# Kernel optimization log

Measured on AMD Instinct MI355X. Metric: run time of the kernel, lower is better.

Reference implementation:

```python
import jax, jax.numpy as jnp
import numpy as np
from jax import lax

B, T, D, V, S = 128, 512, 256, 4096, 512

def setup_inputs() -> dict:
    key = jax.random.key(0)
    ks = jax.random.split(key, 12)
    scale = 1.0 / np.sqrt(D)  # PyTorch RNN default init: U(-1/sqrt(H), 1/sqrt(H))
    inp = {
        "input_ids": jax.random.randint(ks[0], (B, T), 0, V),
        "emb": jax.random.normal(ks[1], (V, D), dtype=jnp.float32) * 0.02,
        "W_ih0": jax.random.uniform(ks[2], (D, D), jnp.float32, -scale, scale),
        "W_hh0": jax.random.uniform(ks[3], (D, D), jnp.float32, -scale, scale),
        "b_ih0": jax.random.uniform(ks[4], (D,), jnp.float32, -scale, scale),
        "b_hh0": jax.random.uniform(ks[5], (D,), jnp.float32, -scale, scale),
        "W_ih1": jax.random.uniform(ks[6], (D, D), jnp.float32, -scale, scale),
        "W_hh1": jax.random.uniform(ks[7], (D, D), jnp.float32, -scale, scale),
        "b_ih1": jax.random.uniform(ks[8], (D,), jnp.float32, -scale, scale),
        "b_hh1": jax.random.uniform(ks[9], (D,), jnp.float32, -scale, scale),
        "W_head": jax.random.normal(ks[10], (S, D), dtype=jnp.float32) * np.sqrt(2.0 / (S + D)),
    }
    return inp

def _rnn_layer(x, W_ih, W_hh, b_ih, b_hh):
    # x: (B, T, D). Elman: h_t = tanh(W_ih x_t + b_ih + W_hh h_{t-1} + b_hh)
    pre = jnp.einsum('btd,hd->bth', x, W_ih) + (b_ih + b_hh)  # batched input GEMM
    def step(h, p):
        h = jnp.tanh(p + h @ W_hh.T)
        return h, h
    h0 = jnp.zeros((x.shape[0], W_hh.shape[0]), dtype=x.dtype)
    _, ys = lax.scan(step, h0, pre.transpose(1, 0, 2))  # scan over T
    return ys.transpose(1, 0, 2)  # (B, T, D)

def reference(input_ids, emb, W_ih0, W_hh0, b_ih0, b_hh0, W_ih1, W_hh1, b_ih1, b_hh1, W_head):
    x = emb[input_ids]                       # (B, T, D); dropout is identity at eval
    h1 = _rnn_layer(x, W_ih0, W_hh0, b_ih0, b_hh0)
    h2 = _rnn_layer(h1, W_ih1, W_hh1, b_ih1, b_hh1)
    logits = jnp.einsum('btd,sd->bts', h2, W_head)  # (B, T, S), head has no bias
    return logits
```

## Files before the change

kernel.cpp:

```cpp
#include <hip/hip_runtime.h>
#include <cstdint>
#include <cstddef>

#define D_DIM 256
#define T_DIM 512
#define B_DIM 128
#define S_DIM 512

typedef __attribute__((ext_vector_type(8))) short short8;
typedef __attribute__((ext_vector_type(4))) float f32x4;

__device__ inline unsigned short f2bf(float x) {
    unsigned u = __builtin_bit_cast(unsigned, x);
    unsigned r = (u + 0x7fffu + ((u >> 16) & 1u)) >> 16;
    return (unsigned short)r;
}
__device__ inline float bf2f(unsigned short b) {
    unsigned u = ((unsigned)b) << 16;
    return __builtin_bit_cast(float, u);
}
__device__ inline float fast_tanh(float x) {
    float ax = __builtin_fabsf(x);
    float e  = __expf(-2.0f * ax);
    float r  = (1.0f - e) * __builtin_amdgcn_rcpf(1.0f + e);
    return __builtin_copysignf(r, x);
}

__device__ inline void split4(float4 v, uint2& hi, uint2& lo) {
    unsigned u0 = __builtin_bit_cast(unsigned, v.x);
    unsigned u1 = __builtin_bit_cast(unsigned, v.y);
    unsigned u2 = __builtin_bit_cast(unsigned, v.z);
    unsigned u3 = __builtin_bit_cast(unsigned, v.w);
    hi.x = (u0 >> 16) | (u1 & 0xFFFF0000u);
    hi.y = (u2 >> 16) | (u3 & 0xFFFF0000u);
    float r0 = v.x - __builtin_bit_cast(float, u0 & 0xFFFF0000u);
    float r1 = v.y - __builtin_bit_cast(float, u1 & 0xFFFF0000u);
    float r2 = v.z - __builtin_bit_cast(float, u2 & 0xFFFF0000u);
    float r3 = v.w - __builtin_bit_cast(float, u3 & 0xFFFF0000u);
    lo.x = (__builtin_bit_cast(unsigned, r0) >> 16)
         | (__builtin_bit_cast(unsigned, r1) & 0xFFFF0000u);
    lo.y = (__builtin_bit_cast(unsigned, r2) >> 16)
         | (__builtin_bit_cast(unsigned, r3) & 0xFFFF0000u);
}

__global__ __launch_bounds__(256, 2)
void gemm_bt_mfma(const float* __restrict__ A, const float* __restrict__ Bm,
                  float* __restrict__ C,
                  const float* __restrict__ bias1, const float* __restrict__ bias2,
                  const int* __restrict__ ids, const float* __restrict__ emb,
                  int M, int N, int K)
{
    __shared__ char smem[65536];

    const int tid  = threadIdx.x;
    const int lane = tid & 63;
    const int quad = lane >> 4;
    const int lcol = lane & 15;
    const int wv   = tid >> 6;
    const int wm   = (wv & 1) * 64;
    const int wn   = (wv >> 1) * 64;
    const int m0   = blockIdx.x * 128;
    const int n0   = blockIdx.y * 128;

    const int rm = tid >> 4;
    const int kq = tid & 15;

    const float* arowp[8];
    const float* browp[8];
#pragma unroll
    for (int i = 0; i < 8; ++i) {
        int gm = m0 + rm + i * 16;
        arowp[i] = ids ? (emb + (size_t)ids[gm] * K) : (A + (size_t)gm * K);
        browp[i] = Bm + (size_t)(n0 + rm + i * 16) * K;
    }
    int woff[8];
#pragma unroll
    for (int i = 0; i < 8; ++i) {
        int m = rm + i * 16;
        woff[i] = (m * 128 + kq * 8) ^ ((m & 7) << 4);
    }

    f32x4 acc[4][4];
#pragma unroll
    for (int mt = 0; mt < 4; ++mt)
#pragma unroll
        for (int nt = 0; nt < 4; ++nt) acc[mt][nt] = (f32x4){0.f, 0.f, 0.f, 0.f};

    float4 pa[8];
#pragma unroll
    for (int i = 0; i < 8; ++i)
        pa[i] = *(const float4*)(arowp[i] + kq * 4);

    for (int it = 0; it < 4; ++it) {
        const int kc = it * 64;
        float4 pb[8];
#pragma unroll
        for (int i = 0; i < 8; ++i)
            pb[i] = *(const float4*)(browp[i] + kc + kq * 4);

        if (it) __syncthreads();

#pragma unroll
        for (int i = 0; i < 8; ++i) {
            uint2 hi, lo;
            split4(pa[i], hi, lo);
            *(uint2*)(smem + 0     + woff[i]) = hi;
            *(uint2*)(smem + 16384 + woff[i]) = lo;
        }
#pragma unroll
        for (int i = 0; i < 8; ++i) {
            uint2 hi, lo;
            split4(pb[i], hi, lo);
            *(uint2*)(smem + 32768 + woff[i]) = hi;
            *(uint2*)(smem + 49152 + woff[i]) = lo;
        }
        __syncthreads();

        if (it < 3) {
#pragma unroll
            for (int i = 0; i < 8; ++i)
                pa[i] = *(const float4*)(arowp[i] + kc + 64 + kq * 4);
        }

#pragma unroll
        for (int ks = 0; ks < 2; ++ks) {
            short8 aHi[4], aLo[4], bHi[4], bLo[4];
#pragma unroll
            for (int mt = 0; mt < 4; ++mt) {
                int m = wm + mt * 16 + lcol;
                int off = (m * 128 + ks * 64 + quad * 16) ^ ((m & 7) << 4);
                aHi[mt] = *(const short8*)(smem + off);
                aLo[mt] = *(const short8*)(smem + 16384 + off);
            }
#pragma unroll
            for (int nt = 0; nt < 4; ++nt) {
                int n = wn + nt * 16 + lcol;
                int off = (n * 128 + ks * 64 + quad * 16) ^ ((n & 7) << 4);
                bHi[nt] = *(const short8*)(smem + 32768 + off);
                bLo[nt] = *(const short8*)(smem + 49152 + off);
            }
#pragma unroll
            for (int mt = 0; mt < 4; ++mt)
#pragma unroll
                for (int nt = 0; nt < 4; ++nt) {
                    acc[mt][nt] = __builtin_amdgcn_mfma_f32_16x16x32_bf16(aHi[mt], bHi[nt], acc[mt][nt], 0, 0, 0);
                    acc[mt][nt] = __builtin_amdgcn_mfma_f32_16x16x32_bf16(aLo[mt], bHi[nt], acc[mt][nt], 0, 0, 0);
                    acc[mt][nt] = __builtin_amdgcn_mfma_f32_16x16x32_bf16(aHi[mt], bLo[nt], acc[mt][nt], 0, 0, 0);
                }
        }
    }

    float bv[4];
#pragma unroll
    for (int nt = 0; nt < 4; ++nt) {
        int gn = n0 + wn + nt * 16 + lcol;
        float v = 0.f;
        if (bias1) v += bias1[gn];
        if (bias2) v += bias2[gn];
        bv[nt] = v;
    }
#pragma unroll
    for (int mt = 0; mt < 4; ++mt) {
        int gmb = m0 + wm + mt * 16 + quad * 4;
#pragma unroll
        for (int r = 0; r < 4; ++r) {
            float* crow = C + (size_t)(gmb + r) * N + n0 + wn;
#pragma unroll
            for (int nt = 0; nt < 4; ++nt)
                crow[nt * 16 + lcol] = acc[mt][nt][r] + bv[nt];
        }
    }
}

__device__ inline void lds_barrier() {
    asm volatile("s_waitcnt lgkmcnt(0)" ::: "memory");
    __builtin_amdgcn_s_barrier();
    __builtin_amdgcn_sched_barrier(0);
}

__global__ __launch_bounds__(512) __attribute__((amdgpu_waves_per_eu(2, 2)))
void rnn_scan_mfma(const float* __restrict__ pre, const float* __restrict__ Whh,
                   float* __restrict__ hout)
{
    const int tid  = threadIdx.x;
    const int wave = tid >> 6;
    const int lane = tid & 63;
    const int quad = lane >> 4;
    const int lcol = lane & 15;
    const int b    = blockIdx.x;

    __shared__ short lds[1024];
    for (int i = tid; i < 1024; i += 512) lds[i] = 0;

    short8 wh[2][8];
#pragma unroll
    for (int tile = 0; tile < 2; ++tile) {
        const int n = wave * 32 + tile * 16 + lcol;
        const float* wr = Whh + (size_t)n * D_DIM + quad * 8;
#pragma unroll
        for (int kt = 0; kt < 8; ++kt) {
            float4 x0 = *(const float4*)(wr + kt * 32);
            float4 x1 = *(const float4*)(wr + kt * 32 + 4);
            float xs[8] = {x0.x, x0.y, x0.z, x0.w, x1.x, x1.y, x1.z, x1.w};
            short8 hi8;
#pragma unroll
            for (int j = 0; j < 8; ++j) hi8[j] = (short)f2bf(xs[j]);
            wh[tile][kt] = hi8;
        }
    }

    const bool active = (lane < 16);
    const int n0 = wave * 32 + lcol;
    const int n1 = n0 + 16;
    const size_t rowbase = (size_t)b * T_DIM * D_DIM;

    const short8 ZS = {0, 0, 0, 0, 0, 0, 0, 0};
    short8 aP[8];
#pragma unroll
    for (int kt = 0; kt < 8; ++kt) aP[kt] = ZS;

    const int aq = quad * 8;

    float pv0 = 0.f, pv1 = 0.f, nv0 = 0.f, nv1 = 0.f;
    if (active) {
        pv0 = pre[rowbase + n0];
        pv1 = pre[rowbase + n1];
        nv0 = pre[rowbase + D_DIM + n0];
        nv1 = pre[rowbase + D_DIM + n1];
    }
    lds_barrier();

    const f32x4 Z = {0.f, 0.f, 0.f, 0.f};

    for (int t = 0; t < T_DIM; ++t) {
        float qv0 = 0.f, qv1 = 0.f;
        if (active && t + 2 < T_DIM) {
            const float* p2 = pre + rowbase + (size_t)(t + 2) * D_DIM;
            qv0 = p2[n0];
            qv1 = p2[n1];
        }

        const int bh = (t & 1) ? 512 : 0;
        if (lcol < 2) {
            const short* pa = lds + bh + lcol * 256 + aq;
#pragma unroll
            for (int kt = 0; kt < 8; ++kt)
                aP[kt] = *(const short8*)(pa + kt * 32);
        }

        f32x4 a1t0, a1t1;
        a1t0 = __builtin_amdgcn_mfma_f32_16x16x32_bf16(aP[0], wh[0][0], Z, 0, 0, 0);
        a1t1 = __builtin_amdgcn_mfma_f32_16x16x32_bf16(aP[0], wh[1][0], Z, 0, 0, 0);
#pragma unroll
        for (int kt = 1; kt < 8; ++kt) {
            a1t0 = __builtin_amdgcn_mfma_f32_16x16x32_bf16(aP[kt], wh[0][kt], a1t0, 0, 0, 0);
            a1t1 = __builtin_amdgcn_mfma_f32_16x16x32_bf16(aP[kt], wh[1][kt], a1t1, 0, 0, 0);
        }

        if (active) {
            const int wH = (t & 1) ? 0 : 512;
            float x0 = a1t0[0] + a1t0[1] + pv0;
            float x1 = a1t1[0] + a1t1[1] + pv1;
            float h0 = fast_tanh(x0);
            float h1 = fast_tanh(x1);
            hout[rowbase + (size_t)t * D_DIM + n0] = h0;
            hout[rowbase + (size_t)t * D_DIM + n1] = h1;
            unsigned short h0h = f2bf(h0);
            unsigned short h0l = f2bf(h0 - bf2f(h0h));
            unsigned short h1h = f2bf(h1);
            unsigned short h1l = f2bf(h1 - bf2f(h1h));
            lds[wH + n0]       = (short)h0h;
            lds[wH + n1]       = (short)h1h;
            lds[wH + 256 + n0] = (short)h0l;
            lds[wH + 256 + n1] = (short)h1l;
        }
        pv0 = nv0; pv1 = nv1;
        nv0 = qv0; nv1 = qv1;
        lds_barrier();
    }
}

extern "C" void kernel_launch(void* const* d_in, const int* in_sizes, int n_in,
                              void* d_out, int out_size, void* d_ws, size_t ws_size,
                              hipStream_t stream)
{
    const int*   ids    = (const int*)  d_in[0];
    const float* emb    = (const float*)d_in[1];
    const float* W_ih0  = (const float*)d_in[2];
    const float* W_hh0  = (const float*)d_in[3];
    const float* b_ih0  = (const float*)d_in[4];
    const float* b_hh0  = (const float*)d_in[5];
    const float* W_ih1  = (const float*)d_in[6];
    const float* W_hh1  = (const float*)d_in[7];
    const float* b_ih1  = (const float*)d_in[8];
    const float* b_hh1  = (const float*)d_in[9];
    const float* W_head = (const float*)d_in[10];

    float* out = (float*)d_out;
    const int M = B_DIM * T_DIM;
    float* pre0 = out;
    float* pre1 = out + (size_t)M * D_DIM;
    float* h1   = (float*)d_ws;
    float* h2   = h1;

    gemm_bt_mfma<<<dim3(M / 128, D_DIM / 128), dim3(256), 0, stream>>>(
        nullptr, W_ih0, pre0, b_ih0, b_hh0, ids, emb, M, D_DIM, D_DIM);
    rnn_scan_mfma<<<dim3(B_DIM), dim3(512), 0, stream>>>(pre0, W_hh0, h1);
    gemm_bt_mfma<<<dim3(M / 128, D_DIM / 128), dim3(256), 0, stream>>>(
        h1, W_ih1, pre1, b_ih1, b_hh1, nullptr, nullptr, M, D_DIM, D_DIM);
    rnn_scan_mfma<<<dim3(B_DIM), dim3(512), 0, stream>>>(pre1, W_hh1, h2);
    gemm_bt_mfma<<<dim3(M / 128, S_DIM / 128), dim3(256), 0, stream>>>(
        h2, W_head, out, nullptr, nullptr, nullptr, nullptr, M, S_DIM, D_DIM);
}
```

Before: 840.0 us.

## Halve GEMM k-chunk for higher occupancy and split recurrent MFMA chains

```diff
diff --git a/kernel.cpp b/kernel.cpp
--- a/kernel.cpp
+++ b/kernel.cpp
@@ -43,14 +43,14 @@
          | (__builtin_bit_cast(unsigned, r3) & 0xFFFF0000u);
 }
 
-__global__ __launch_bounds__(256, 2)
+__global__ __launch_bounds__(256, 3)
 void gemm_bt_mfma(const float* __restrict__ A, const float* __restrict__ Bm,
                   float* __restrict__ C,
                   const float* __restrict__ bias1, const float* __restrict__ bias2,
                   const int* __restrict__ ids, const float* __restrict__ emb,
                   int M, int N, int K)
 {
-    __shared__ char smem[65536];
+    __shared__ char smem[32768];
 
     const int tid  = threadIdx.x;
     const int lane = tid & 63;
@@ -62,23 +62,16 @@
     const int m0   = blockIdx.x * 128;
     const int n0   = blockIdx.y * 128;
 
-    const int rm = tid >> 4;
-    const int kq = tid & 15;
-
-    const float* arowp[8];
-    const float* browp[8];
-#pragma unroll
-    for (int i = 0; i < 8; ++i) {
-        int gm = m0 + rm + i * 16;
-        arowp[i] = ids ? (emb + (size_t)ids[gm] * K) : (A + (size_t)gm * K);
-        browp[i] = Bm + (size_t)(n0 + rm + i * 16) * K;
-    }
-    int woff[8];
-#pragma unroll
-    for (int i = 0; i < 8; ++i) {
-        int m = rm + i * 16;
-        woff[i] = (m * 128 + kq * 8) ^ ((m & 7) << 4);
-    }
+    const int rs = tid >> 1;
+    const int hf = tid & 1;
+    const int gmA = m0 + rs;
+    const float* arow = (ids ? (emb + (size_t)ids[gmA] * K)
+                             : (A + (size_t)gmA * K)) + hf * 16;
+    const float* brow = Bm + (size_t)(n0 + rs) * K + hf * 16;
+
+    const int swz = ((rs >> 1) & 3) << 4;
+    const int ws0 = rs * 64 + (((hf * 2)     << 4) ^ swz);
+    const int ws1 = rs * 64 + (((hf * 2 + 1) << 4) ^ swz);
 
     f32x4 acc[4][4];
 #pragma unroll
@@ -86,68 +79,70 @@
 #pragma unroll
         for (int nt = 0; nt < 4; ++nt) acc[mt][nt] = (f32x4){0.f, 0.f, 0.f, 0.f};
 
-    float4 pa[8];
-#pragma unroll
-    for (int i = 0; i < 8; ++i)
-        pa[i] = *(const float4*)(arowp[i] + kq * 4);
-
-    for (int it = 0; it < 4; ++it) {
-        const int kc = it * 64;
-        float4 pb[8];
-#pragma unroll
-        for (int i = 0; i < 8; ++i)
-            pb[i] = *(const float4*)(browp[i] + kc + kq * 4);
+    float4 pa0 = *(const float4*)(arow + 0);
+    float4 pa1 = *(const float4*)(arow + 4);
+    float4 pa2 = *(const float4*)(arow + 8);
+    float4 pa3 = *(const float4*)(arow + 12);
+
+    for (int it = 0; it < 8; ++it) {
+        const int kc = it * 32;
+        float4 pb0 = *(const float4*)(brow + kc + 0);
+        float4 pb1 = *(const float4*)(brow + kc + 4);
+        float4 pb2 = *(const float4*)(brow + kc + 8);
+        float4 pb3 = *(const float4*)(brow + kc + 12);
 
         if (it) __syncthreads();
 
-#pragma unroll
-        for (int i = 0; i < 8; ++i) {
-            uint2 hi, lo;
-            split4(pa[i], hi, lo);
-            *(uint2*)(smem + 0     + woff[i]) = hi;
-            *(uint2*)(smem + 16384 + woff[i]) = lo;
-        }
-#pragma unroll
-        for (int i = 0; i < 8; ++i) {
-            uint2 hi, lo;
-            split4(pb[i], hi, lo);
-            *(uint2*)(smem + 32768 + woff[i]) = hi;
-            *(uint2*)(smem + 49152 + woff[i]) = lo;
+        {
+            uint2 h0, l0, h1, l1, h2, l2, h3, l3;
+            split4(pa0, h0, l0); split4(pa1, h1, l1);
+            split4(pa2, h2, l2); split4(pa3, h3, l3);
+            *(uint4*)(smem + 0    + ws0) = make_uint4(h0.x, h0.y, h1.x, h1.y);
+            *(uint4*)(smem + 0    + ws1) = make_uint4(h2.x, h2.y, h3.x, h3.y);
+            *(uint4*)(smem + 8192 + ws0) = make_uint4(l0.x, l0.y, l1.x, l1.y);
+            *(uint4*)(smem + 8192 + ws1) = make_uint4(l2.x, l2.y, l3.x, l3.y);
+        }
+        {
+            uint2 h0, l0, h1, l1, h2, l2, h3, l3;
+            split4(pb0, h0, l0); split4(pb1, h1, l1);
+            split4(pb2, h2, l2); split4(pb3, h3, l3);
+            *(uint4*)(smem + 16384 + ws0) = make_uint4(h0.x, h0.y, h1.x, h1.y);
+            *(uint4*)(smem + 16384 + ws1) = make_uint4(h2.x, h2.y, h3.x, h3.y);
+            *(uint4*)(smem + 24576 + ws0) = make_uint4(l0.x, l0.y, l1.x, l1.y);
+            *(uint4*)(smem + 24576 + ws1) = make_uint4(l2.x, l2.y, l3.x, l3.y);
         }
         __syncthreads();
 
-        if (it < 3) {
-#pragma unroll
-            for (int i = 0; i < 8; ++i)
-                pa[i] = *(const float4*)(arowp[i] + kc + 64 + kq * 4);
-        }
-
-#pragma unroll
-        for (int ks = 0; ks < 2; ++ks) {
-            short8 aHi[4], aLo[4], bHi[4], bLo[4];
-#pragma unroll
-            for (int mt = 0; mt < 4; ++mt) {
-                int m = wm + mt * 16 + lcol;
-                int off = (m * 128 + ks * 64 + quad * 16) ^ ((m & 7) << 4);
-                aHi[mt] = *(const short8*)(smem + off);
-                aLo[mt] = *(const short8*)(smem + 16384 + off);
+        if (it < 7) {
+            pa0 = *(const float4*)(arow + kc + 32);
+            pa1 = *(const float4*)(arow + kc + 36);
+            pa2 = *(const float4*)(arow + kc + 40);
+            pa3 = *(const float4*)(arow + kc + 44);
+        }
+
+        short8 aHi[4], aLo[4], bHi[4], bLo[4];
+#pragma unroll
+        for (int mt = 0; mt < 4; ++mt) {
+            int m = wm + mt * 16 + lcol;
+            int off = m * 64 + ((quad * 16) ^ ((((m >> 1) & 3)) << 4));
+            aHi[mt] = *(const short8*)(smem + off);
+            aLo[mt] = *(const short8*)(smem + 8192 + off);
+        }
+#pragma unroll
+        for (int nt = 0; nt < 4; ++nt) {
+            int n = wn + nt * 16 + lcol;
+            int off = n * 64 + ((quad * 16) ^ ((((n >> 1) & 3)) << 4));
+            bHi[nt] = *(const short8*)(smem + 16384 + off);
+            bLo[nt] = *(const short8*)(smem + 24576 + off);
+        }
+#pragma unroll
+        for (int mt = 0; mt < 4; ++mt)
+#pragma unroll
+            for (int nt = 0; nt < 4; ++nt) {
+                acc[mt][nt] = __builtin_amdgcn_mfma_f32_16x16x32_bf16(aHi[mt], bHi[nt], acc[mt][nt], 0, 0, 0);
+                acc[mt][nt] = __builtin_amdgcn_mfma_f32_16x16x32_bf16(aLo[mt], bHi[nt], acc[mt][nt], 0, 0, 0);
+                acc[mt][nt] = __builtin_amdgcn_mfma_f32_16x16x32_bf16(aHi[mt], bLo[nt], acc[mt][nt], 0, 0, 0);
             }
-#pragma unroll
-            for (int nt = 0; nt < 4; ++nt) {
-                int n = wn + nt * 16 + lcol;
-                int off = (n * 128 + ks * 64 + quad * 16) ^ ((n & 7) << 4);
-                bHi[nt] = *(const short8*)(smem + 32768 + off);
-                bLo[nt] = *(const short8*)(smem + 49152 + off);
-            }
-#pragma unroll
-            for (int mt = 0; mt < 4; ++mt)
-#pragma unroll
-                for (int nt = 0; nt < 4; ++nt) {
-                    acc[mt][nt] = __builtin_amdgcn_mfma_f32_16x16x32_bf16(aHi[mt], bHi[nt], acc[mt][nt], 0, 0, 0);
-                    acc[mt][nt] = __builtin_amdgcn_mfma_f32_16x16x32_bf16(aLo[mt], bHi[nt], acc[mt][nt], 0, 0, 0);
-                    acc[mt][nt] = __builtin_amdgcn_mfma_f32_16x16x32_bf16(aHi[mt], bLo[nt], acc[mt][nt], 0, 0, 0);
-                }
-        }
     }
 
     float bv[4];
@@ -248,23 +243,25 @@
                 aP[kt] = *(const short8*)(pa + kt * 32);
         }
 
-        f32x4 a1t0, a1t1;
-        a1t0 = __builtin_amdgcn_mfma_f32_16x16x32_bf16(aP[0], wh[0][0], Z, 0, 0, 0);
-        a1t1 = __builtin_amdgcn_mfma_f32_16x16x32_bf16(aP[0], wh[1][0], Z, 0, 0, 0);
-#pragma unroll
-        for (int kt = 1; kt < 8; ++kt) {
-            a1t0 = __builtin_amdgcn_mfma_f32_16x16x32_bf16(aP[kt], wh[0][kt], a1t0, 0, 0, 0);
-            a1t1 = __builtin_amdgcn_mfma_f32_16x16x32_bf16(aP[kt], wh[1][kt], a1t1, 0, 0, 0);
+        f32x4 c0t0, c1t0, c0t1, c1t1;
+        c0t0 = __builtin_amdgcn_mfma_f32_16x16x32_bf16(aP[0], wh[0][0], Z, 0, 0, 0);
+        c0t1 = __builtin_amdgcn_mfma_f32_16x16x32_bf16(aP[0], wh[1][0], Z, 0, 0, 0);
+        c1t0 = __builtin_amdgcn_mfma_f32_16x16x32_bf16(aP[4], wh[0][4], Z, 0, 0, 0);
+        c1t1 = __builtin_amdgcn_mfma_f32_16x16x32_bf16(aP[4], wh[1][4], Z, 0, 0, 0);
+#pragma unroll
+        for (int kt = 1; kt < 4; ++kt) {
+            c0t0 = __builtin_amdgcn_mfma_f32_16x16x32_bf16(aP[kt],     wh[0][kt],     c0t0, 0, 0, 0);
+            c0t1 = __builtin_amdgcn_mfma_f32_16x16x32_bf16(aP[kt],     wh[1][kt],     c0t1, 0, 0, 0);
+            c1t0 = __builtin_amdgcn_mfma_f32_16x16x32_bf16(aP[kt + 4], wh[0][kt + 4], c1t0, 0, 0, 0);
+            c1t1 = __builtin_amdgcn_mfma_f32_16x16x32_bf16(aP[kt + 4], wh[1][kt + 4], c1t1, 0, 0, 0);
         }
 
         if (active) {
             const int wH = (t & 1) ? 0 : 512;
-            float x0 = a1t0[0] + a1t0[1] + pv0;
-            float x1 = a1t1[0] + a1t1[1] + pv1;
+            float x0 = (c0t0[0] + c1t0[0]) + (c0t0[1] + c1t0[1]) + pv0;
+            float x1 = (c0t1[0] + c1t1[0]) + (c0t1[1] + c1t1[1]) + pv1;
             float h0 = fast_tanh(x0);
             float h1 = fast_tanh(x1);
-            hout[rowbase + (size_t)t * D_DIM + n0] = h0;
-            hout[rowbase + (size_t)t * D_DIM + n1] = h1;
             unsigned short h0h = f2bf(h0);
             unsigned short h0l = f2bf(h0 - bf2f(h0h));
             unsigned short h1h = f2bf(h1);
@@ -273,6 +270,8 @@
             lds[wH + n1]       = (short)h1h;
             lds[wH + 256 + n0] = (short)h0l;
             lds[wH + 256 + n1] = (short)h1l;
+            hout[rowbase + (size_t)t * D_DIM + n0] = h0;
+            hout[rowbase + (size_t)t * D_DIM + n1] = h1;
         }
         pv0 = nv0; pv1 = nv1;
         nv0 = qv0; nv1 = qv1;
```

Measured after the change: 831.7 us. About the same (-1.0%).
